# Kernel optimization log

Hardware: AMD Instinct MI355X
Metric: run time of the kernel (lower is better)

The kernel has to match this reference:

```python
import jax, jax.numpy as jnp
import numpy as np

D_MODEL = 1024
N_HEADS = 16
HEAD_DIM = D_MODEL // N_HEADS
SPARSITY = 0.5  # torch.rand(...) < sparsity_factor -> True means masked (disallowed)


def setup_inputs() -> dict:
    key = jax.random.key(0)
    ks = jax.random.split(key, 12)
    B, S, D = 2, 2048, D_MODEL
    query = jax.random.normal(ks[0], (B, S, D), dtype=jnp.float32)
    key_t = jax.random.normal(ks[1], (B, S, D), dtype=jnp.float32)
    value = jax.random.normal(ks[2], (B, S, D), dtype=jnp.float32)
    # per-forward random boolean mask, materialized deterministically here
    mask = jax.random.uniform(ks[3], (B, S, S)) < SPARSITY
    scale = 1.0 / np.sqrt(D)
    Wq = jax.random.uniform(ks[4], (D, D), jnp.float32, -scale, scale)
    Wk = jax.random.uniform(ks[5], (D, D), jnp.float32, -scale, scale)
    Wv = jax.random.uniform(ks[6], (D, D), jnp.float32, -scale, scale)
    Wo = jax.random.uniform(ks[7], (D, D), jnp.float32, -scale, scale)
    bq = jnp.zeros((D,), jnp.float32)
    bk = jnp.zeros((D,), jnp.float32)
    bv = jnp.zeros((D,), jnp.float32)
    bo = jnp.zeros((D,), jnp.float32)
    return {"query": query, "key": key_t, "value": value, "mask": mask,
            "Wq": Wq, "Wk": Wk, "Wv": Wv, "Wo": Wo,
            "bq": bq, "bk": bk, "bv": bv, "bo": bo}


def reference(query, key, value, mask, Wq, Wk, Wv, Wo, bq, bk, bv, bo):
    B, S, D = query.shape
    H, hd = N_HEADS, HEAD_DIM
    # in-projections (torch uses x @ W.T + b)
    q = (query @ Wq.T + bq).reshape(B, S, H, hd).transpose(0, 2, 1, 3)  # (B,H,S,hd)
    k = (key @ Wk.T + bk).reshape(B, S, H, hd).transpose(0, 2, 1, 3)
    v = (value @ Wv.T + bv).reshape(B, S, H, hd).transpose(0, 2, 1, 3)
    scores = jnp.einsum('bhqd,bhkd->bhqk', q, k) / jnp.sqrt(jnp.float32(hd))
    # bool mask: True = disallowed; broadcast over heads
    scores = jnp.where(mask[:, None, :, :], -jnp.inf, scores)
    attn = jax.nn.softmax(scores, axis=-1)  # dropout inactive at eval
    out = jnp.einsum('bhqk,bhkd->bhqd', attn, v)  # (B,H,S,hd)
    out = out.transpose(0, 2, 1, 3).reshape(B, S, D)
    return out @ Wo.T + bo
```

## Files before the change

kernel.cpp:

```cpp
#include <hip/hip_runtime.h>
#include <stdint.h>

#define MTOK   4096
#define DMODEL 1024
#define SEQ    2048
#define NH     16
#define HD     64
#define LDP    68
#define QSCL   0.18033688f
#define NWORDS (2 * SEQ * SEQ / 64)

typedef _Float16 h8  __attribute__((ext_vector_type(8)));
typedef _Float16 h4  __attribute__((ext_vector_type(4)));
typedef _Float16 h2  __attribute__((ext_vector_type(2)));
typedef __fp16   fp16x2 __attribute__((ext_vector_type(2)));
typedef float    f16v __attribute__((ext_vector_type(16)));
typedef float    f4  __attribute__((ext_vector_type(4)));
typedef int      iv4 __attribute__((ext_vector_type(4)));

typedef __attribute__((address_space(1))) const unsigned int g_u32;
typedef __attribute__((address_space(3))) unsigned int       l_u32;

__device__ __forceinline__ void g2l16(const void* g, void* l) {
    __builtin_amdgcn_global_load_lds((g_u32*)(unsigned long long)g,
                                     (l_u32*)(unsigned int)(unsigned long long)l,
                                     16, 0, 0);
}

__device__ __forceinline__ h2 pkrtz(float a, float b) {
    fp16x2 r = __builtin_amdgcn_cvt_pkrtz(a, b);
    return __builtin_bit_cast(h2, r);
}

#if __has_builtin(__builtin_amdgcn_exp2f)
#define E2(x) __builtin_amdgcn_exp2f(x)
#else
#define E2(x) exp2f(x)
#endif

__device__ __forceinline__ float dot2sum(int v, float acc) {
    h2 a = __builtin_bit_cast(h2, v);
#if __has_builtin(__builtin_amdgcn_fdot2)
    h2 one2 = {(_Float16)1.0f, (_Float16)1.0f};
    return __builtin_amdgcn_fdot2(a, one2, acc, false);
#else
    return acc + (float)a.x + (float)a.y;
#endif
}

__global__ __launch_bounds__(256) void prep_kernel(
    const float* __restrict__ s0, const float* __restrict__ s1,
    const float* __restrict__ s2, const float* __restrict__ s3,
    const float* __restrict__ s4, const float* __restrict__ s5,
    const float* __restrict__ s6,
    _Float16* __restrict__ d0, _Float16* __restrict__ d1,
    _Float16* __restrict__ d2, _Float16* __restrict__ d3,
    _Float16* __restrict__ d4, _Float16* __restrict__ d5,
    _Float16* __restrict__ d6,
    const unsigned char* __restrict__ mb, const unsigned int* __restrict__ mu,
    unsigned long long* __restrict__ mout) {
    const int z = blockIdx.y;
    const int gid = blockIdx.x * 256 + threadIdx.x;
    const int stride = gridDim.x * 256;
    if (z < 7) {
        const float* s = (z == 0) ? s0 : (z == 1) ? s1 : (z == 2) ? s2
                       : (z == 3) ? s3 : (z == 4) ? s4 : (z == 5) ? s5 : s6;
        _Float16* d = (z == 0) ? d0 : (z == 1) ? d1 : (z == 2) ? d2
                    : (z == 3) ? d3 : (z == 4) ? d4 : (z == 5) ? d5 : d6;
        const int n4 = (z < 3) ? (MTOK * DMODEL / 4) : (DMODEL * DMODEL / 4);
        for (int i = gid; i < n4; i += stride) {
            float4 v = ((const float4*)s)[i];
            h4 o = {(_Float16)v.x, (_Float16)v.y, (_Float16)v.z, (_Float16)v.w};
            ((h4*)d)[i] = o;
        }
    } else {
        __shared__ int wsum[4];
        int cnt = 0;
        const uchar4* mp4 = (const uchar4*)mb;
#pragma unroll
        for (int i = 0; i < 8; ++i) {
            uchar4 v = mp4[threadIdx.x * 8 + i];
            cnt += (v.x != 0) + (v.y != 0) + (v.z != 0) + (v.w != 0);
        }
#pragma unroll
        for (int off = 32; off > 0; off >>= 1) cnt += __shfl_down(cnt, off, 64);
        if ((threadIdx.x & 63) == 0) wsum[threadIdx.x >> 6] = cnt;
        __syncthreads();
        const int byteflag = (wsum[0] + wsum[1] + wsum[2] + wsum[3]) > 2500;

        for (int w = gid; w < NWORDS; w += stride) {
            unsigned long long bits = 0ull;
            if (byteflag) {
                const uint4* p = (const uint4*)(mb + (size_t)w * 64);
#pragma unroll
                for (int i = 0; i < 4; ++i) {
                    uint4 v = p[i];
                    unsigned dw[4] = {v.x, v.y, v.z, v.w};
#pragma unroll
                    for (int j = 0; j < 4; ++j) {
                        unsigned d = dw[j];
                        unsigned nib = (unsigned)((d & 0xFFu) != 0)
                                     | ((unsigned)((d & 0xFF00u) != 0) << 1)
                                     | ((unsigned)((d & 0xFF0000u) != 0) << 2)
                                     | ((unsigned)((d >> 24) != 0) << 3);
                        bits |= (unsigned long long)nib << (i * 16 + j * 4);
                    }
                }
            } else {
                const uint4* p = (const uint4*)(mu + (size_t)w * 64);
#pragma unroll
                for (int i = 0; i < 16; ++i) {
                    uint4 v = p[i];
                    unsigned nib = (unsigned)(v.x != 0u)
                                 | ((unsigned)(v.y != 0u) << 1)
                                 | ((unsigned)(v.z != 0u) << 2)
                                 | ((unsigned)(v.w != 0u) << 3);
                    bits |= (unsigned long long)nib << (i * 4);
                }
            }
            mout[w] = bits;
        }
    }
}

template <int MODE, int BM, int BN>
__device__ __forceinline__ void gemm16_body(const _Float16* __restrict__ A,
                                            const _Float16* __restrict__ W,
                                            const float* __restrict__ bias,
                                            void* __restrict__ outv,
                                            float scale) {
    __shared__ __align__(16) _Float16 Asb[BM * 64];
    __shared__ __align__(16) _Float16 Bsb[BN * 64];
    constexpr int NI = BM / 32, NJ = BN / 32;
    constexpr int WM = BM / 2,  WN = BN / 2;
    constexpr int RA = BM * 128 / 4096;
    constexpr int RB = BN * 128 / 4096;
    const int tid = threadIdx.x;
    const int wv = tid >> 6, lane = tid & 63;
    const int l15 = lane & 15, g = lane >> 4;
    const int wy = wv >> 1, wx = wv & 1;
    const int m0 = blockIdx.x * BM, n0 = blockIdx.y * BN;

    f4 acc[NI][NJ];
#pragma unroll
    for (int i = 0; i < NI; ++i)
#pragma unroll
        for (int j = 0; j < NJ; ++j) acc[i][j] = (f4){0.f, 0.f, 0.f, 0.f};

    const char* Ab = (const char*)A;
    const char* Wb = (const char*)W;
    int srowA[RA], scolA[RA];
#pragma unroll
    for (int r = 0; r < RA; ++r) {
        const int o = (r * 256 + tid) * 16;
        srowA[r] = o >> 7;
        scolA[r] = (((o >> 4) & 7) ^ (srowA[r] & 7)) * 16;
    }
    int srowB[RB], scolB[RB];
#pragma unroll
    for (int r = 0; r < RB; ++r) {
        const int o = (r * 256 + tid) * 16;
        srowB[r] = o >> 7;
        scolB[r] = (((o >> 4) & 7) ^ (srowB[r] & 7)) * 16;
    }

    for (int kt = 0; kt < 16; ++kt) {
        const int k0b = kt * 128;
        __syncthreads();
#pragma unroll
        for (int r = 0; r < RA; ++r)
            g2l16(Ab + (size_t)(m0 + srowA[r]) * 2048 + k0b + scolA[r],
                  (char*)Asb + (r * 256 + tid) * 16);
#pragma unroll
        for (int r = 0; r < RB; ++r)
            g2l16(Wb + (size_t)(n0 + srowB[r]) * 2048 + k0b + scolB[r],
                  (char*)Bsb + (r * 256 + tid) * 16);
        __syncthreads();

#pragma unroll
        for (int ksub = 0; ksub < 2; ++ksub) {
            h8 af[NI], bf[NJ];
#pragma unroll
            for (int t = 0; t < NI; ++t) {
                const int row = wy * WM + t * 16 + l15;
                const int pos = (ksub * 4 + g) ^ (row & 7);
                af[t] = *(const h8*)(Asb + row * 64 + pos * 8);
            }
#pragma unroll
            for (int t = 0; t < NJ; ++t) {
                const int row = wx * WN + t * 16 + l15;
                const int pos = (ksub * 4 + g) ^ (row & 7);
                bf[t] = *(const h8*)(Bsb + row * 64 + pos * 8);
            }
#pragma unroll
            for (int i = 0; i < NI; ++i)
#pragma unroll
                for (int j = 0; j < NJ; ++j) {
                    if (MODE == 2)
                        acc[i][j] = __builtin_amdgcn_mfma_f32_16x16x32_f16(
                            bf[j], af[i], acc[i][j], 0, 0, 0);
                    else
                        acc[i][j] = __builtin_amdgcn_mfma_f32_16x16x32_f16(
                            af[i], bf[j], acc[i][j], 0, 0, 0);
                }
        }
    }

#pragma unroll
    for (int j = 0; j < NJ; ++j) {
#pragma unroll
        for (int i = 0; i < NI; ++i) {
            if (MODE == 2) {
                const int m = m0 + wy * WM + i * 16 + l15;
                const int b = m >> 11, s = m & 2047;
#pragma unroll
                for (int r = 0; r < 4; ++r) {
                    const int n = n0 + wx * WN + j * 16 + g * 4 + r;
                    const int h = n >> 6, d = n & 63;
                    ((_Float16*)outv)[(((size_t)(b * NH + h)) * HD + d) * SEQ + s] =
                        (_Float16)(acc[i][j][r] + bias[n]);
                }
            } else {
                const int n = n0 + wx * WN + j * 16 + l15;
                const float bb = bias[n];
                const int mbase = m0 + wy * WM + i * 16 + g * 4;
                if (MODE == 1) {
                    const int h = n >> 6, d = n & 63;
#pragma unroll
                    for (int r = 0; r < 4; ++r) {
                        const int m = mbase + r;
                        const int b = m >> 11, s = m & 2047;
                        ((_Float16*)outv)[(((size_t)(b * NH + h)) * SEQ + s) * HD + d] =
                            (_Float16)((acc[i][j][r] + bb) * scale);
                    }
                } else {
#pragma unroll
                    for (int r = 0; r < 4; ++r)
                        ((float*)outv)[(size_t)(mbase + r) * DMODEL + n] =
                            acc[i][j][r] + bb;
                }
            }
        }
    }
}

__global__ __launch_bounds__(256) void qkv_gemm16_kernel(
    const _Float16* __restrict__ xq, const _Float16* __restrict__ xk,
    const _Float16* __restrict__ xv,
    const _Float16* __restrict__ Wq, const _Float16* __restrict__ Wk,
    const _Float16* __restrict__ Wv,
    const float* __restrict__ bq, const float* __restrict__ bk,
    const float* __restrict__ bv,
    _Float16* __restrict__ q_out, _Float16* __restrict__ k_out,
    _Float16* __restrict__ vt_out) {
    const int z = blockIdx.z;
    if (z == 0)      gemm16_body<1, 128, 128>(xq, Wq, bq, (void*)q_out, QSCL);
    else if (z == 1) gemm16_body<1, 128, 128>(xk, Wk, bk, (void*)k_out, 1.0f);
    else             gemm16_body<2, 128, 128>(xv, Wv, bv, (void*)vt_out, 1.0f);
}

__global__ __launch_bounds__(256) void out_gemm16_kernel(
    const _Float16* __restrict__ X, const _Float16* __restrict__ W,
    const float* __restrict__ bias, float* __restrict__ out) {
    gemm16_body<0, 64, 128>(X, W, bias, (void*)out, 1.0f);
}

__global__ __launch_bounds__(512, 4) void attn_kernel(
    const _Float16* __restrict__ Q, const _Float16* __restrict__ K,
    const _Float16* __restrict__ Vt,
    const unsigned long long* __restrict__ mbits,
    _Float16* __restrict__ out) {
    __shared__ __align__(16) _Float16 shm[32768 + 64];

    const int tid = threadIdx.x;
    const int wv = tid >> 6, lane = tid & 63;
    const int grp = wv >> 2, wvg = wv & 3;
    const int l31 = lane & 31, hi = lane >> 5;
    const int q0 = blockIdx.x * 128;
    const int bh = blockIdx.y;
    const int b = bh >> 4, h = bh & 15;
    const size_t bho = (size_t)bh * (SEQ * HD);
    const int qrow = q0 + wvg * 32 + l31;

    if (tid < 16) {
        unsigned mlo = (tid & 1 ? 0u : 0xFFFFu) | (tid & 2 ? 0u : 0xFFFF0000u);
        unsigned mhi = (tid & 4 ? 0u : 0xFFFFu) | (tid & 8 ? 0u : 0xFFFF0000u);
        ((uint2*)&shm[32768])[tid] = (uint2){mlo, mhi};
    }

    h8 qf[4];
    const _Float16* qp = Q + bho + (size_t)qrow * HD;
#pragma unroll
    for (int ks = 0; ks < 4; ++ks) qf[ks] = *(const h8*)(qp + ks * 16 + hi * 8);

    f16v Ot[2];
#pragma unroll
    for (int mt = 0; mt < 2; ++mt)
#pragma unroll
        for (int r = 0; r < 16; ++r) Ot[mt][r] = 0.f;
    float l_r = 0.f;

    const int cA = wvg, cB = wvg + 4;
    const _Float16* kg = K + bho;
    const _Float16* vg = Vt + bho;
    const _Float16* klp = kg + (size_t)(grp * 64 + lane) * HD;
    const _Float16* vlp = vg + (size_t)lane * SEQ + grp * 64;
    const unsigned long long* mrow =
        mbits + ((size_t)b * SEQ + qrow) * (SEQ / 64);

    _Float16* KTb = &shm[grp * 8192];
    _Float16* VTb = &shm[16384 + grp * 8192];

#define STAGE(buf) do {                                                     \
    char* kd = (char*)(KTb + (buf) * 4096);                                 \
    char* vd = (char*)(VTb + (buf) * 4096);                                 \
    g2l16(klp + cA * 8, kd + cA * 1024);                                    \
    g2l16(klp + cB * 8, kd + cB * 1024);                                    \
    g2l16(vlp + cA * 8, vd + cA * 1024);                                    \
    g2l16(vlp + cB * 8, vd + cB * 1024);                                    \
    klp += 128 * HD; vlp += 128;                                            \
} while (0)

    uint2 mw = *(const uint2*)(mrow + grp);
    STAGE(0);
    __syncthreads();

    const uint2* lut = (const uint2*)&shm[32768];
    int rp[8][2];

    for (int it = 0; it < 16; ++it) {
        const int cur = it & 1;
        const int kt = 2 * it + grp;
        uint2 mwn;
        if (it < 15) {
            STAGE(cur ^ 1);
            mwn = *(const uint2*)(mrow + kt + 2);
        }
        const _Float16* Kc = KTb + cur * 4096;
        const _Float16* Vc = VTb + cur * 4096;

        f16v sc0, sc1;
#pragma unroll
        for (int r = 0; r < 16; ++r) { sc0[r] = 0.f; sc1[r] = 0.f; }
        __builtin_amdgcn_s_setprio(1);
#pragma unroll
        for (int ks = 0; ks < 4; ++ks) {
            const int po = (2 * ks + hi) * 512;
            h8 kf0 = *(const h8*)(Kc + po + l31 * 8);
            h8 kf1 = *(const h8*)(Kc + po + (32 + l31) * 8);
            sc0 = __builtin_amdgcn_mfma_f32_32x32x16_f16(kf0, qf[ks], sc0, 0, 0, 0);
            sc1 = __builtin_amdgcn_mfma_f32_32x32x16_f16(kf1, qf[ks], sc1, 0, 0, 0);
        }
        __builtin_amdgcn_s_setprio(0);

#pragma unroll
        for (int mt = 0; mt < 2; ++mt) {
            const unsigned w = mt ? mw.y : mw.x;
            const unsigned wl = w >> (hi * 4);
            const f16v& s = mt ? sc1 : sc0;
#pragma unroll
            for (int g4 = 0; g4 < 4; ++g4) {
                const uint2 m2 = lut[(wl >> (g4 * 8)) & 15u];
                float p0 = E2(s[g4 * 4 + 0]);
                float p1 = E2(s[g4 * 4 + 1]);
                float p2 = E2(s[g4 * 4 + 2]);
                float p3 = E2(s[g4 * 4 + 3]);
                rp[mt * 4 + g4][0] =
                    __builtin_bit_cast(int, pkrtz(p0, p1)) & (int)m2.x;
                rp[mt * 4 + g4][1] =
                    __builtin_bit_cast(int, pkrtz(p2, p3)) & (int)m2.y;
            }
        }

        float l0 = 0.f, l1 = 0.f;
#pragma unroll
        for (int ks = 0; ks < 4; ++ks) {
            int a0 = rp[2 * ks][0], a1 = rp[2 * ks][1];
            int b0 = rp[2 * ks + 1][0], b1 = rp[2 * ks + 1][1];
            asm volatile("v_permlane32_swap_b32 %0, %1" : "+v"(a0), "+v"(b0));
            asm volatile("v_permlane32_swap_b32 %0, %1" : "+v"(a1), "+v"(b1));
            l0 = dot2sum(a0, l0); l1 = dot2sum(a1, l1);
            l0 = dot2sum(b0, l0); l1 = dot2sum(b1, l1);
            iv4 pi = {a0, a1, b0, b1};
            h8 pf = __builtin_bit_cast(h8, pi);
            const int po = (2 * ks + hi) * 512;
            h8 vf0 = *(const h8*)(Vc + po + l31 * 8);
            h8 vf1 = *(const h8*)(Vc + po + (32 + l31) * 8);
            __builtin_amdgcn_s_setprio(1);
            Ot[0] = __builtin_amdgcn_mfma_f32_32x32x16_f16(vf0, pf, Ot[0], 0, 0, 0);
            Ot[1] = __builtin_amdgcn_mfma_f32_32x32x16_f16(vf1, pf, Ot[1], 0, 0, 0);
            __builtin_amdgcn_s_setprio(0);
        }
        l_r += l0 + l1;

        if (it < 15) mw = mwn;
        __syncthreads();
    }
#undef STAGE

    l_r += __shfl_xor(l_r, 32);
    float* mrg = (float*)&shm[0];
    float* lm  = mrg + 128 * LDP;
    const int ql = wvg * 32 + l31;
    if (grp == 1) {
#pragma unroll
        for (int mt = 0; mt < 2; ++mt)
#pragma unroll
            for (int t = 0; t < 4; ++t) {
                f4 v = {Ot[mt][t * 4 + 0], Ot[mt][t * 4 + 1],
                        Ot[mt][t * 4 + 2], Ot[mt][t * 4 + 3]};
                *(f4*)&mrg[ql * LDP + mt * 32 + t * 8 + hi * 4] = v;
            }
        if (hi == 0) lm[ql] = l_r;
    }
    __syncthreads();
    if (grp == 0) {
        l_r += lm[ql];
        const float inv = 1.0f / l_r;
        _Float16* op = out + ((size_t)b * SEQ + qrow) * DMODEL + h * HD;
#pragma unroll
        for (int mt = 0; mt < 2; ++mt)
#pragma unroll
            for (int t = 0; t < 4; ++t) {
                const int d = mt * 32 + t * 8 + hi * 4;
                f4 v = *(const f4*)&mrg[ql * LDP + d];
                h4 ov = {(_Float16)((Ot[mt][t * 4 + 0] + v.x) * inv),
                         (_Float16)((Ot[mt][t * 4 + 1] + v.y) * inv),
                         (_Float16)((Ot[mt][t * 4 + 2] + v.z) * inv),
                         (_Float16)((Ot[mt][t * 4 + 3] + v.w) * inv)};
                *(h4*)(op + d) = ov;
            }
    }
}

extern "C" void kernel_launch(void* const* d_in, const int* in_sizes, int n_in,
                              void* d_out, int out_size, void* d_ws, size_t ws_size,
                              hipStream_t stream) {
    const float* query = (const float*)d_in[0];
    const float* key_  = (const float*)d_in[1];
    const float* value = (const float*)d_in[2];
    const void*  mask  = d_in[3];
    const float* Wq = (const float*)d_in[4];
    const float* Wk = (const float*)d_in[5];
    const float* Wv = (const float*)d_in[6];
    const float* Wo = (const float*)d_in[7];
    const float* bq = (const float*)d_in[8];
    const float* bk = (const float*)d_in[9];
    const float* bv = (const float*)d_in[10];
    const float* bo = (const float*)d_in[11];

    char* ws = (char*)d_ws;
    _Float16* xq  = (_Float16*)(ws + 256);
    _Float16* xk  = xq + (size_t)MTOK * DMODEL;
    _Float16* xv  = xk + (size_t)MTOK * DMODEL;
    _Float16* Wqh = xv + (size_t)MTOK * DMODEL;
    _Float16* Wkh = Wqh + (size_t)DMODEL * DMODEL;
    _Float16* Wvh = Wkh + (size_t)DMODEL * DMODEL;
    _Float16* Woh = Wvh + (size_t)DMODEL * DMODEL;
    _Float16* q_ws  = Woh + (size_t)DMODEL * DMODEL;
    _Float16* k_ws  = q_ws + (size_t)MTOK * DMODEL;
    _Float16* vt_ws = k_ws + (size_t)MTOK * DMODEL;
    _Float16* a_ws  = vt_ws + (size_t)MTOK * DMODEL;
    unsigned long long* mb_ws =
        (unsigned long long*)(a_ws + (size_t)MTOK * DMODEL);

    prep_kernel<<<dim3(1024, 8), 256, 0, stream>>>(
        query, key_, value, Wq, Wk, Wv, Wo, xq, xk, xv, Wqh, Wkh, Wvh, Woh,
        (const unsigned char*)mask, (const unsigned int*)mask, mb_ws);

    dim3 gqkv(MTOK / 128, DMODEL / 128, 3);
    qkv_gemm16_kernel<<<gqkv, 256, 0, stream>>>(xq, xk, xv, Wqh, Wkh, Wvh,
                                                bq, bk, bv, q_ws, k_ws, vt_ws);

    dim3 gattn(SEQ / 128, 2 * NH);
    attn_kernel<<<gattn, 512, 0, stream>>>(q_ws, k_ws, vt_ws, mb_ws, a_ws);

    dim3 gout(MTOK / 64, DMODEL / 128);
    out_gemm16_kernel<<<gout, 256, 0, stream>>>(a_ws, Woh, bo, (float*)d_out);
}
```

Measured before the change: 273.9 us.

## Write K and V pre-swizzled in LDS tile layout and remap attention block order

The QKV projection now writes K and V directly in the blocked layout that the attention kernel's shared-memory tiles use. This lets the attention stage copy each tile with contiguous 16-byte global-to-LDS loads instead of strided row gathers. The attention grid is also remapped so that consecutive blocks fall on different (batch, head) pairs, a change to cache and scheduling locality. The cost is scattered 2-byte stores in the GEMM epilogue, and correctness now depends on the projection and attention kernels agreeing on the custom layout.

```diff
diff --git a/kernel.cpp b/kernel.cpp
--- a/kernel.cpp
+++ b/kernel.cpp
@@ -196,7 +196,7 @@
             for (int i = 0; i < NI; ++i)
 #pragma unroll
                 for (int j = 0; j < NJ; ++j) {
-                    if (MODE == 2)
+                    if (MODE == 4)
                         acc[i][j] = __builtin_amdgcn_mfma_f32_16x16x32_f16(
                             bf[j], af[i], acc[i][j], 0, 0, 0);
                     else
@@ -210,14 +210,15 @@
     for (int j = 0; j < NJ; ++j) {
 #pragma unroll
         for (int i = 0; i < NI; ++i) {
-            if (MODE == 2) {
+            if (MODE == 4) {
                 const int m = m0 + wy * WM + i * 16 + l15;
                 const int b = m >> 11, s = m & 2047;
+                const int koff = (s >> 6) * 4096 + ((s >> 3) & 7) * 512 + (s & 7);
 #pragma unroll
                 for (int r = 0; r < 4; ++r) {
                     const int n = n0 + wx * WN + j * 16 + g * 4 + r;
                     const int h = n >> 6, d = n & 63;
-                    ((_Float16*)outv)[(((size_t)(b * NH + h)) * HD + d) * SEQ + s] =
+                    ((_Float16*)outv)[(size_t)(b * NH + h) * 131072 + koff + d * 8] =
                         (_Float16)(acc[i][j][r] + bias[n]);
                 }
             } else {
@@ -232,6 +233,17 @@
                         const int b = m >> 11, s = m & 2047;
                         ((_Float16*)outv)[(((size_t)(b * NH + h)) * SEQ + s) * HD + d] =
                             (_Float16)((acc[i][j][r] + bb) * scale);
+                    }
+                } else if (MODE == 3) {
+                    const int h = n >> 6, d = n & 63;
+                    const int doff = (d >> 3) * 512 + (d & 7);
+#pragma unroll
+                    for (int r = 0; r < 4; ++r) {
+                        const int m = mbase + r;
+                        const int b = m >> 11, s = m & 2047;
+                        ((_Float16*)outv)[(size_t)(b * NH + h) * 131072 +
+                                          (s >> 6) * 4096 + doff + (s & 63) * 8] =
+                            (_Float16)(acc[i][j][r] + bb);
                     }
                 } else {
 #pragma unroll
@@ -255,8 +267,8 @@
     _Float16* __restrict__ vt_out) {
     const int z = blockIdx.z;
     if (z == 0)      gemm16_body<1, 128, 128>(xq, Wq, bq, (void*)q_out, QSCL);
-    else if (z == 1) gemm16_body<1, 128, 128>(xk, Wk, bk, (void*)k_out, 1.0f);
-    else             gemm16_body<2, 128, 128>(xv, Wv, bv, (void*)vt_out, 1.0f);
+    else if (z == 1) gemm16_body<3, 128, 128>(xk, Wk, bk, (void*)k_out, 1.0f);
+    else             gemm16_body<4, 128, 128>(xv, Wv, bv, (void*)vt_out, 1.0f);
 }
 
 __global__ __launch_bounds__(256) void out_gemm16_kernel(
@@ -266,8 +278,8 @@
 }
 
 __global__ __launch_bounds__(512, 4) void attn_kernel(
-    const _Float16* __restrict__ Q, const _Float16* __restrict__ K,
-    const _Float16* __restrict__ Vt,
+    const _Float16* __restrict__ Q, const _Float16* __restrict__ Ksw,
+    const _Float16* __restrict__ Vsw,
     const unsigned long long* __restrict__ mbits,
     _Float16* __restrict__ out) {
     __shared__ __align__(16) _Float16 shm[32768 + 64];
@@ -276,8 +288,10 @@
     const int wv = tid >> 6, lane = tid & 63;
     const int grp = wv >> 2, wvg = wv & 3;
     const int l31 = lane & 31, hi = lane >> 5;
-    const int q0 = blockIdx.x * 128;
-    const int bh = blockIdx.y;
+    const int lin = blockIdx.x + 16 * blockIdx.y;
+    const int swz = (lin & 7) * 64 + (lin >> 3);
+    const int bh = swz >> 4;
+    const int q0 = (swz & 15) * 128;
     const int b = bh >> 4, h = bh & 15;
     const size_t bho = (size_t)bh * (SEQ * HD);
     const int qrow = q0 + wvg * 32 + l31;
@@ -300,11 +314,9 @@
         for (int r = 0; r < 16; ++r) Ot[mt][r] = 0.f;
     float l_r = 0.f;
 
-    const int cA = wvg, cB = wvg + 4;
-    const _Float16* kg = K + bho;
-    const _Float16* vg = Vt + bho;
-    const _Float16* klp = kg + (size_t)(grp * 64 + lane) * HD;
-    const _Float16* vlp = vg + (size_t)lane * SEQ + grp * 64;
+    const int gtid = tid & 255;
+    const _Float16* ksrc = Ksw + bho + grp * 4096 + gtid * 8;
+    const _Float16* vsrc = Vsw + bho + grp * 4096 + gtid * 8;
     const unsigned long long* mrow =
         mbits + ((size_t)b * SEQ + qrow) * (SEQ / 64);
 
@@ -314,11 +326,11 @@
 #define STAGE(buf) do {                                                     \
     char* kd = (char*)(KTb + (buf) * 4096);                                 \
     char* vd = (char*)(VTb + (buf) * 4096);                                 \
-    g2l16(klp + cA * 8, kd + cA * 1024);                                    \
-    g2l16(klp + cB * 8, kd + cB * 1024);                                    \
-    g2l16(vlp + cA * 8, vd + cA * 1024);                                    \
-    g2l16(vlp + cB * 8, vd + cB * 1024);                                    \
-    klp += 128 * HD; vlp += 128;                                            \
+    g2l16(ksrc,        kd + gtid * 16);                                     \
+    g2l16(ksrc + 2048, kd + 4096 + gtid * 16);                              \
+    g2l16(vsrc,        vd + gtid * 16);                                     \
+    g2l16(vsrc + 2048, vd + 4096 + gtid * 16);                              \
+    ksrc += 8192; vsrc += 8192;                                             \
 } while (0)
 
     uint2 mw = *(const uint2*)(mrow + grp);
@@ -347,7 +359,7 @@
         for (int ks = 0; ks < 4; ++ks) {
             const int po = (2 * ks + hi) * 512;
             h8 kf0 = *(const h8*)(Kc + po + l31 * 8);
-            h8 kf1 = *(const h8*)(Kc + po + (32 + l31) * 8);
+            h8 kf1 = *(const h8*)(Kc + po + 256 + l31 * 8);
             sc0 = __builtin_amdgcn_mfma_f32_32x32x16_f16(kf0, qf[ks], sc0, 0, 0, 0);
             sc1 = __builtin_amdgcn_mfma_f32_32x32x16_f16(kf1, qf[ks], sc1, 0, 0, 0);
         }
@@ -385,7 +397,7 @@
             h8 pf = __builtin_bit_cast(h8, pi);
             const int po = (2 * ks + hi) * 512;
             h8 vf0 = *(const h8*)(Vc + po + l31 * 8);
-            h8 vf1 = *(const h8*)(Vc + po + (32 + l31) * 8);
+            h8 vf1 = *(const h8*)(Vc + po + 256 + l31 * 8);
             __builtin_amdgcn_s_setprio(1);
             Ot[0] = __builtin_amdgcn_mfma_f32_32x32x16_f16(vf0, pf, Ot[0], 0, 0, 0);
             Ot[1] = __builtin_amdgcn_mfma_f32_32x32x16_f16(vf1, pf, Ot[1], 0, 0, 0);
```

Result: slower. 285.3 us (+4.2%).
